# Kernel optimization log

Measured on AMD Instinct MI355X. Metric: run time of the kernel, lower is better.

Reference implementation:

```python
import jax, jax.numpy as jnp
import numpy as np

V, D, B, L = 433, 120, 4096, 16  # vocab, d_model, batch, seq_len
H4 = 4 * D
LN_EPS = 1e-5


def setup_inputs() -> dict:
    key = jax.random.key(0)
    ks = jax.random.split(key, 12)
    s = 1.0 / np.sqrt(D)  # PyTorch LSTM init range
    u = lambda k, shape: jax.random.uniform(k, shape, jnp.float32, -s, s)
    return {
        "x": jax.random.randint(ks[0], (B, L), 0, V, dtype=jnp.int32),
        "embed": jax.random.normal(ks[1], (V, D), jnp.float32) * 0.02,
        "Wih0": u(ks[2], (H4, D)), "Whh0": u(ks[3], (H4, D)),
        "bih0": u(ks[4], (H4,)), "bhh0": u(ks[5], (H4,)),
        "Wih1": u(ks[6], (H4, D)), "Whh1": u(ks[7], (H4, D)),
        "bih1": u(ks[8], (H4,)), "bhh1": u(ks[9], (H4,)),
        "gamma": jnp.ones((D,), jnp.float32),
        "beta": jnp.zeros((D,), jnp.float32),
    }


def _lstm_layer(x, Wih, Whh, bih, bhh):
    """One LSTM layer, batch_first input [B,L,D] -> [B,L,H]. PyTorch gate order i,f,g,o."""
    b, _, _ = x.shape
    h_dim = Whh.shape[1]
    # Precompute input contribution for all timesteps in one big GEMM.
    xg = jnp.einsum('bld,gd->blg', x, Wih) + bih + bhh  # [B,L,4H]

    def step(carry, g_t):
        h, c = carry
        gates = g_t + h @ Whh.T  # [B,4H]
        i, f, g, o = jnp.split(gates, 4, axis=-1)
        c = jax.nn.sigmoid(f) * c + jax.nn.sigmoid(i) * jnp.tanh(g)
        h = jax.nn.sigmoid(o) * jnp.tanh(c)
        return (h, c), h

    init = (jnp.zeros((b, h_dim), x.dtype), jnp.zeros((b, h_dim), x.dtype))
    _, hs = jax.lax.scan(step, init, jnp.swapaxes(xg, 0, 1))  # [L,B,H]
    return jnp.swapaxes(hs, 0, 1)


def _layernorm(h, gamma, beta):
    mu = jnp.mean(h, axis=-1, keepdims=True)
    var = jnp.mean(jnp.square(h - mu), axis=-1, keepdims=True)
    return (h - mu) / jnp.sqrt(var + LN_EPS) * gamma + beta


def reference(x, embed, Wih0, Whh0, bih0, bhh0, Wih1, Whh1, bih1, bhh1, gamma, beta):
    h = embed[x]                               # [B,L,D] token embedding
    h = _lstm_layer(h, Wih0, Whh0, bih0, bhh0)  # layer 0
    h = _lstm_layer(h, Wih1, Whh1, bih1, bhh1)  # layer 1
    out = _layernorm(h, gamma, beta)
    logits = jnp.einsum('bld,vd->blv', out, embed)  # tied-embedding head (no bias)
    return logits
```

## Files before the change

### kernel.cpp

```cpp
#include <hip/hip_runtime.h>


#define VSZ 433
#define DIM 120
#define BSZ 4096
#define SEQ 16
#define H4  480
#define MTOT (BSZ*SEQ)
#define KP  128
#define NPAD 448
#define TB  16
#define GP  484
#define HP  136

typedef unsigned int   u32;
typedef unsigned short u16;
typedef __attribute__((ext_vector_type(8))) short    v8bf;
typedef __attribute__((ext_vector_type(8))) _Float16 v8h;
typedef __attribute__((ext_vector_type(4))) float    v4f;

__device__ __forceinline__ float bf2f(u16 u){ union{u32 i;float f;}z; z.i=((u32)u)<<16; return z.f; }
__device__ __forceinline__ u16 f2bf(float f){
  union{float f;u32 u;}z; z.f=f;
  u32 u = z.u + 0x7fffu + ((z.u>>16)&1u);
  return (u16)(u>>16);
}

#define EW_OFF   0u
#define B1S_OFF  831488u
#define EMBP_OFF 833408u
#define HB0_OFF  948096u
#define H1N_OFF  17725312u

__global__ __launch_bounds__(512) void k_ew(const float* __restrict__ embed,
                                            const float* __restrict__ Wih0,
                                            const float* __restrict__ bih0,
                                            const float* __restrict__ bhh0,
                                            float* __restrict__ EW)
{
  __shared__ float e[DIM];
  const int v = blockIdx.x, tid = threadIdx.x;
  if (tid < DIM) e[tid] = embed[v*DIM + tid];
  __syncthreads();
  if (tid < H4) {
    float acc = bih0[tid] + bhh0[tid];
    #pragma unroll
    for (int k0 = 0; k0 < DIM; k0 += 4) {
      float4 w = *(const float4*)(Wih0 + tid*DIM + k0);
      acc = fmaf(e[k0+0], w.x, acc);
      acc = fmaf(e[k0+1], w.y, acc);
      acc = fmaf(e[k0+2], w.z, acc);
      acc = fmaf(e[k0+3], w.w, acc);
    }
    EW[v*H4 + tid] = acc;
  }
}

__global__ __launch_bounds__(256) void k_prep2(const float* __restrict__ embed,
                                               const float* __restrict__ bih1,
                                               const float* __restrict__ bhh1,
                                               u16* __restrict__ embP,
                                               float* __restrict__ b1s)
{
  const int idx = blockIdx.x*256 + threadIdx.x;
  if (idx < NPAD*KP) {
    int n = idx >> 7, k = idx & 127;
    embP[idx] = (n < VSZ && k < DIM) ? f2bf(embed[n*DIM + k]) : (u16)0;
  } else if (idx < NPAD*KP + H4) {
    int g = idx - NPAD*KP;
    b1s[g] = bih1[g] + bhh1[g];
  }
}

__global__ __launch_bounds__(512) void k_rec0(const float* __restrict__ Whh,
                                              const float* __restrict__ EW,
                                              const int* __restrict__ x,
                                              _Float16* __restrict__ hb0)
{
  __shared__ float gLs[TB][GP];
  __shared__ __align__(16) _Float16 hLh[TB][HP];
  __shared__ int xL[TB*SEQ];

  const int tid  = threadIdx.x;
  const int wave = tid >> 6, lane = tid & 63;
  const int cl   = lane & 15, quad = lane >> 4;
  const int b0   = blockIdx.x * TB;

  for (int i = tid; i < TB*SEQ; i += 512) xL[i] = x[b0*SEQ + i];
  for (int i = tid; i < TB*HP; i += 512) (&hLh[0][0])[i] = (_Float16)0.f;
  __syncthreads();

  v8h Bf[4][4];
  #pragma unroll
  for (int i = 0; i < 4; ++i) {
    const int nt = wave*4 + i;
    const bool vld = (nt < 30);
    const int n = vld ? nt*16 + cl : 0;
    #pragma unroll
    for (int kt = 0; kt < 4; ++kt) {
      const int k0 = kt*32 + quad*8;
      v8h f = {0,0,0,0,0,0,0,0};
      if (vld && k0 < DIM) {
        float4 q0 = *(const float4*)(Whh + n*DIM + k0);
        float4 q1 = *(const float4*)(Whh + n*DIM + k0 + 4);
        f[0]=(_Float16)q0.x; f[1]=(_Float16)q0.y; f[2]=(_Float16)q0.z; f[3]=(_Float16)q0.w;
        f[4]=(_Float16)q1.x; f[5]=(_Float16)q1.y; f[6]=(_Float16)q1.z; f[7]=(_Float16)q1.w;
      }
      Bf[i][kt] = f;
    }
  }

  float srcv[4][4];
  auto load_src = [&](int t) {
    #pragma unroll
    for (int i = 0; i < 4; ++i) {
      const int nt = wave*4 + i;
      if (nt < 30) {
        const int n = nt*16 + cl;
        #pragma unroll
        for (int r = 0; r < 4; ++r)
          srcv[i][r] = EW[(size_t)xL[(quad*4 + r)*SEQ + t]*H4 + n];
      }
    }
  };
  load_src(0);

  const int d  = tid % 120;
  const int rg = tid / 120;
  float C[4] = {0.f, 0.f, 0.f, 0.f};

  for (int t = 0; t < SEQ; ++t) {
    __syncthreads();
    v8h Af[4];
    #pragma unroll
    for (int kt = 0; kt < 4; ++kt)
      Af[kt] = *(const v8h*)&hLh[cl][kt*32 + quad*8];
    v4f acc[4];
    #pragma unroll
    for (int i = 0; i < 4; ++i) {
      acc[i][0]=srcv[i][0]; acc[i][1]=srcv[i][1];
      acc[i][2]=srcv[i][2]; acc[i][3]=srcv[i][3];
    }
    #pragma unroll
    for (int i = 0; i < 4; ++i)
      if (wave*4 + i < 30) {
        #pragma unroll
        for (int kt = 0; kt < 4; ++kt)
          acc[i] = __builtin_amdgcn_mfma_f32_16x16x32_f16(Af[kt], Bf[i][kt], acc[i], 0, 0, 0);
      }
    if (t + 1 < SEQ) load_src(t + 1);
    #pragma unroll
    for (int i = 0; i < 4; ++i) {
      const int nt = wave*4 + i;
      if (nt < 30) {
        #pragma unroll
        for (int r = 0; r < 4; ++r)
          gLs[quad*4 + r][nt*16 + cl] = acc[i][r];
      }
    }
    __syncthreads();
    if (tid < 480) {
      #pragma unroll
      for (int r = 0; r < 4; ++r) {
        const int row = rg*4 + r;
        const float gi = gLs[row][d      ];
        const float gf = gLs[row][d + 120];
        const float gg = gLs[row][d + 240];
        const float go = gLs[row][d + 360];
        const float si = 1.f / (1.f + __expf(-gi));
        const float sf = 1.f / (1.f + __expf(-gf));
        const float tg = 1.f - 2.f / (__expf(2.f*gg) + 1.f);
        const float so = 1.f / (1.f + __expf(-go));
        const float c  = sf * C[r] + si * tg;
        C[r] = c;
        const float tc = 1.f - 2.f / (__expf(2.f*c) + 1.f);
        const float h  = so * tc;
        hLh[row][d] = (_Float16)h;
        hb0[((size_t)t*BSZ + b0 + row)*KP + d] = (_Float16)h;
      }
    } else {
      const int i = tid - 480;
      #pragma unroll
      for (int j = 0; j < 4; ++j) {
        const int idx = i*4 + j, row = idx >> 3, col = 120 + (idx & 7);
        hb0[((size_t)t*BSZ + b0 + row)*KP + col] = (_Float16)0.f;
      }
    }
  }
}

__global__ __launch_bounds__(512) void k_rec1(const float* __restrict__ Wih1,
                                              const float* __restrict__ Whh1,
                                              const float* __restrict__ b1s,
                                              const _Float16* __restrict__ hb0,
                                              const float* __restrict__ gamma,
                                              const float* __restrict__ beta,
                                              u16* __restrict__ h1n)
{
  __shared__ float gLs[TB][GP];
  __shared__ __align__(16) _Float16 hLh[TB][HP];

  const int tid  = threadIdx.x;
  const int wave = tid >> 6, lane = tid & 63;
  const int cl   = lane & 15, quad = lane >> 4;
  const int b0   = blockIdx.x * TB;

  for (int i = tid; i < TB*HP; i += 512) (&hLh[0][0])[i] = (_Float16)0.f;

  v8h Bi[4][4], Bh[4][4];
  float bias[4];
  #pragma unroll
  for (int i = 0; i < 4; ++i) {
    const int nt = wave*4 + i;
    const bool vld = (nt < 30);
    const int n = vld ? nt*16 + cl : 0;
    bias[i] = vld ? b1s[n] : 0.f;
    #pragma unroll
    for (int kt = 0; kt < 4; ++kt) {
      const int k0 = kt*32 + quad*8;
      v8h fi = {0,0,0,0,0,0,0,0}, fh = {0,0,0,0,0,0,0,0};
      if (vld && k0 < DIM) {
        float4 q0 = *(const float4*)(Wih1 + n*DIM + k0);
        float4 q1 = *(const float4*)(Wih1 + n*DIM + k0 + 4);
        fi[0]=(_Float16)q0.x; fi[1]=(_Float16)q0.y; fi[2]=(_Float16)q0.z; fi[3]=(_Float16)q0.w;
        fi[4]=(_Float16)q1.x; fi[5]=(_Float16)q1.y; fi[6]=(_Float16)q1.z; fi[7]=(_Float16)q1.w;
        float4 p0 = *(const float4*)(Whh1 + n*DIM + k0);
        float4 p1 = *(const float4*)(Whh1 + n*DIM + k0 + 4);
        fh[0]=(_Float16)p0.x; fh[1]=(_Float16)p0.y; fh[2]=(_Float16)p0.z; fh[3]=(_Float16)p0.w;
        fh[4]=(_Float16)p1.x; fh[5]=(_Float16)p1.y; fh[6]=(_Float16)p1.z; fh[7]=(_Float16)p1.w;
      }
      Bi[i][kt] = fi;
      Bh[i][kt] = fh;
    }
  }

  const int d  = tid % 120;
  const int rg = tid / 120;
  const float gmm = (tid < 480) ? gamma[d] : 0.f;
  const float bta = (tid < 480) ? beta[d]  : 0.f;
  float C[4] = {0.f, 0.f, 0.f, 0.f};
  __syncthreads();

  for (int t = 0; t < SEQ; ++t) {
    v8h A0[4], A1[4];
    #pragma unroll
    for (int kt = 0; kt < 4; ++kt)
      A0[kt] = *(const v8h*)&hb0[((size_t)t*BSZ + b0 + cl)*KP + kt*32 + quad*8];
    #pragma unroll
    for (int kt = 0; kt < 4; ++kt)
      A1[kt] = *(const v8h*)&hLh[cl][kt*32 + quad*8];
    v4f acc[4];
    #pragma unroll
    for (int i = 0; i < 4; ++i)
      acc[i] = (v4f){bias[i], bias[i], bias[i], bias[i]};
    #pragma unroll
    for (int i = 0; i < 4; ++i)
      if (wave*4 + i < 30) {
        #pragma unroll
        for (int kt = 0; kt < 4; ++kt) {
          acc[i] = __builtin_amdgcn_mfma_f32_16x16x32_f16(A0[kt], Bi[i][kt], acc[i], 0, 0, 0);
          acc[i] = __builtin_amdgcn_mfma_f32_16x16x32_f16(A1[kt], Bh[i][kt], acc[i], 0, 0, 0);
        }
      }
    #pragma unroll
    for (int i = 0; i < 4; ++i) {
      const int nt = wave*4 + i;
      if (nt < 30) {
        #pragma unroll
        for (int r = 0; r < 4; ++r)
          gLs[quad*4 + r][nt*16 + cl] = acc[i][r];
      }
    }
    __syncthreads();
    float hreg[4];
    if (tid < 480) {
      #pragma unroll
      for (int r = 0; r < 4; ++r) {
        const int row = rg*4 + r;
        const float gi = gLs[row][d      ];
        const float gf = gLs[row][d + 120];
        const float gg = gLs[row][d + 240];
        const float go = gLs[row][d + 360];
        const float si = 1.f / (1.f + __expf(-gi));
        const float sf = 1.f / (1.f + __expf(-gf));
        const float tg = 1.f - 2.f / (__expf(2.f*gg) + 1.f);
        const float so = 1.f / (1.f + __expf(-go));
        const float c  = sf * C[r] + si * tg;
        C[r] = c;
        const float tc = 1.f - 2.f / (__expf(2.f*c) + 1.f);
        const float h  = so * tc;
        hreg[r] = h;
        hLh[row][d] = (_Float16)h;
        gLs[row][d] = h;
      }
    }
    __syncthreads();
    if (tid < 128) {
      const int row = tid >> 3, seg = tid & 7;
      float s1 = 0.f, s2 = 0.f;
      #pragma unroll
      for (int j = 0; j < 15; ++j) {
        const float v = gLs[row][seg*15 + j];
        s1 += v; s2 = fmaf(v, v, s2);
      }
      gLs[row][464 + seg] = s1;
      gLs[row][472 + seg] = s2;
    }
    __syncthreads();
    if (tid < 16) {
      float s1 = 0.f, s2 = 0.f;
      #pragma unroll
      for (int j = 0; j < 8; ++j) { s1 += gLs[tid][464 + j]; s2 += gLs[tid][472 + j]; }
      const float mu = s1 * (1.f/DIM);
      const float var = s2 * (1.f/DIM) - mu*mu;
      gLs[tid][480] = mu;
      gLs[tid][481] = rsqrtf(var + 1e-5f);
    }
    __syncthreads();
    if (tid < 480) {
      #pragma unroll
      for (int r = 0; r < 4; ++r) {
        const int row = rg*4 + r;
        const float mu = gLs[row][480], rs = gLs[row][481];
        const float v = fmaf((hreg[r] - mu)*rs, gmm, bta);
        h1n[((size_t)(b0 + row)*SEQ + t)*KP + d] = f2bf(v);
      }
    } else {
      const int i = tid - 480;
      #pragma unroll
      for (int j = 0; j < 4; ++j) {
        const int idx = i*4 + j, row = idx >> 3, col = 120 + (idx & 7);
        h1n[((size_t)(b0 + row)*SEQ + t)*KP + col] = (u16)0;
      }
    }
    __syncthreads();
  }
}

__global__ __launch_bounds__(256) void k_head(const u16* __restrict__ A,
                                              const u16* __restrict__ Bp,
                                              float* __restrict__ out)
{
  const int wv = threadIdx.x >> 6, lane = threadIdx.x & 63;
  const int cl = lane & 15, quad = lane >> 4;
  const int mtb = (blockIdx.x*4 + wv)*4;
  v8bf a[4][4];
  #pragma unroll
  for (int i = 0; i < 4; ++i)
    #pragma unroll
    for (int kt = 0; kt < 4; ++kt)
      a[i][kt] = *(const v8bf*)&A[((size_t)(mtb+i)*16 + cl)*KP + kt*32 + quad*8];
  for (int nt = 0; nt < NPAD/16; ++nt) {
    const int n = nt*16 + cl;
    v8bf bfr[4];
    #pragma unroll
    for (int kt = 0; kt < 4; ++kt)
      bfr[kt] = *(const v8bf*)&Bp[(size_t)n*KP + kt*32 + quad*8];
    #pragma unroll
    for (int i = 0; i < 4; ++i) {
      v4f acc = {0.f, 0.f, 0.f, 0.f};
      #pragma unroll
      for (int kt = 0; kt < 4; ++kt)
        acc = __builtin_amdgcn_mfma_f32_16x16x32_bf16(a[i][kt], bfr[kt], acc, 0, 0, 0);
      if (n < VSZ) {
        #pragma unroll
        for (int r = 0; r < 4; ++r)
          out[(size_t)((mtb+i)*16 + quad*4 + r)*VSZ + n] = acc[r];
      }
    }
  }
}

extern "C" void kernel_launch(void* const* d_in, const int* in_sizes, int n_in,
                              void* d_out, int out_size, void* d_ws, size_t ws_size,
                              hipStream_t stream)
{
  (void)in_sizes; (void)n_in; (void)out_size; (void)ws_size;
  const int*   x     = (const int*)d_in[0];
  const float* embed = (const float*)d_in[1];
  const float* Wih0  = (const float*)d_in[2];
  const float* Whh0  = (const float*)d_in[3];
  const float* bih0  = (const float*)d_in[4];
  const float* bhh0  = (const float*)d_in[5];
  const float* Wih1  = (const float*)d_in[6];
  const float* Whh1  = (const float*)d_in[7];
  const float* bih1  = (const float*)d_in[8];
  const float* bhh1  = (const float*)d_in[9];
  const float* gamma = (const float*)d_in[10];
  const float* beta  = (const float*)d_in[11];

  char* ws = (char*)d_ws;
  float*     EW   = (float*)(ws + EW_OFF);
  float*     b1s  = (float*)(ws + B1S_OFF);
  u16*       embP = (u16*)(ws + EMBP_OFF);
  _Float16*  hb0  = (_Float16*)(ws + HB0_OFF);
  u16*       h1n  = (u16*)(ws + H1N_OFF);

  k_ew   <<<VSZ, 512, 0, stream>>>(embed, Wih0, bih0, bhh0, EW);
  k_prep2<<<226, 256, 0, stream>>>(embed, bih1, bhh1, embP, b1s);
  k_rec0 <<<BSZ/TB, 512, 0, stream>>>(Whh0, EW, x, hb0);
  k_rec1 <<<BSZ/TB, 512, 0, stream>>>(Wih1, Whh1, b1s, hb0, gamma, beta, h1n);
  k_head <<<MTOT/256, 256, 0, stream>>>(h1n, embP, (float*)d_out);
}
```

Measured before the change: 296.0 us.

## Remap gate math to per-wave rows and use warp-shuffle LayerNorm reduction

Both recurrent kernels now give each wave two batch rows, with each lane handling two hidden units using float2 LDS reads and packed half stores. In layer 1 the LayerNorm statistics are reduced with wave-level xor shuffles instead of an LDS tree, which removes three block barriers per timestep. The next timestep's layer-0 hidden input is also prefetched into registers ahead of the MFMAs. This aims to cut synchronisation and LDS traffic in the serial timestep loop, at the cost of more registers.

```diff
diff --git a/kernel.cpp b/kernel.cpp
--- a/kernel.cpp
+++ b/kernel.cpp
@@ -25,6 +25,11 @@
   u32 u = z.u + 0x7fffu + ((z.u>>16)&1u);
   return (u16)(u>>16);
 }
+__device__ __forceinline__ u32 packh2(float a, float b){
+  union{_Float16 h[2]; u32 u;} z;
+  z.h[0] = (_Float16)a; z.h[1] = (_Float16)b;
+  return z.u;
+}
 
 #define EW_OFF   0u
 #define B1S_OFF  831488u
@@ -125,9 +130,10 @@
   };
   load_src(0);
 
-  const int d  = tid % 120;
-  const int rg = tid / 120;
-  float C[4] = {0.f, 0.f, 0.f, 0.f};
+  const int prow = wave*2;
+  const bool act = lane < 60;
+  const int d0   = lane*2;
+  float C[2][2] = {{0.f,0.f},{0.f,0.f}};
 
   for (int t = 0; t < SEQ; ++t) {
     __syncthreads();
@@ -159,31 +165,32 @@
       }
     }
     __syncthreads();
-    if (tid < 480) {
-      #pragma unroll
-      for (int r = 0; r < 4; ++r) {
-        const int row = rg*4 + r;
-        const float gi = gLs[row][d      ];
-        const float gf = gLs[row][d + 120];
-        const float gg = gLs[row][d + 240];
-        const float go = gLs[row][d + 360];
-        const float si = 1.f / (1.f + __expf(-gi));
-        const float sf = 1.f / (1.f + __expf(-gf));
-        const float tg = 1.f - 2.f / (__expf(2.f*gg) + 1.f);
-        const float so = 1.f / (1.f + __expf(-go));
-        const float c  = sf * C[r] + si * tg;
-        C[r] = c;
-        const float tc = 1.f - 2.f / (__expf(2.f*c) + 1.f);
-        const float h  = so * tc;
-        hLh[row][d] = (_Float16)h;
-        hb0[((size_t)t*BSZ + b0 + row)*KP + d] = (_Float16)h;
-      }
-    } else {
-      const int i = tid - 480;
-      #pragma unroll
-      for (int j = 0; j < 4; ++j) {
-        const int idx = i*4 + j, row = idx >> 3, col = 120 + (idx & 7);
-        hb0[((size_t)t*BSZ + b0 + row)*KP + col] = (_Float16)0.f;
+    #pragma unroll
+    for (int rr = 0; rr < 2; ++rr) {
+      const int row = prow + rr;
+      if (act) {
+        const float2 gi = *(const float2*)&gLs[row][d0      ];
+        const float2 gf = *(const float2*)&gLs[row][d0 + 120];
+        const float2 gg = *(const float2*)&gLs[row][d0 + 240];
+        const float2 go = *(const float2*)&gLs[row][d0 + 360];
+        float h2[2];
+        #pragma unroll
+        for (int k = 0; k < 2; ++k) {
+          const float vi = k ? gi.y : gi.x, vf = k ? gf.y : gf.x;
+          const float vg = k ? gg.y : gg.x, vo = k ? go.y : go.x;
+          const float si = 1.f / (1.f + __expf(-vi));
+          const float sf = 1.f / (1.f + __expf(-vf));
+          const float tg = 1.f - 2.f / (__expf(2.f*vg) + 1.f);
+          const float so = 1.f / (1.f + __expf(-vo));
+          const float c  = sf * C[rr][k] + si * tg;
+          C[rr][k] = c;
+          const float tc = 1.f - 2.f / (__expf(2.f*c) + 1.f);
+          h2[k] = so * tc;
+        }
+        *(u32*)&hLh[row][d0] = packh2(h2[0], h2[1]);
+        *(u32*)&hb0[((size_t)t*BSZ + b0 + row)*KP + d0] = packh2(h2[0], h2[1]);
+      } else {
+        *(u32*)&hb0[((size_t)t*BSZ + b0 + row)*KP + 120 + 2*(lane - 60)] = 0u;
       }
     }
   }
@@ -234,21 +241,34 @@
     }
   }
 
-  const int d  = tid % 120;
-  const int rg = tid / 120;
-  const float gmm = (tid < 480) ? gamma[d] : 0.f;
-  const float bta = (tid < 480) ? beta[d]  : 0.f;
-  float C[4] = {0.f, 0.f, 0.f, 0.f};
+  const int prow = wave*2;
+  const bool act = lane < 60;
+  const int d0   = lane*2;
+  float gmm[2] = {0.f, 0.f}, bta[2] = {0.f, 0.f};
+  if (act) {
+    gmm[0] = gamma[d0]; gmm[1] = gamma[d0+1];
+    bta[0] = beta[d0];  bta[1] = beta[d0+1];
+  }
+  float C[2][2] = {{0.f,0.f},{0.f,0.f}};
+
+  v8h A0n[4];
+  #pragma unroll
+  for (int kt = 0; kt < 4; ++kt)
+    A0n[kt] = *(const v8h*)&hb0[((size_t)0*BSZ + b0 + cl)*KP + kt*32 + quad*8];
   __syncthreads();
 
   for (int t = 0; t < SEQ; ++t) {
-    v8h A0[4], A1[4];
-    #pragma unroll
-    for (int kt = 0; kt < 4; ++kt)
-      A0[kt] = *(const v8h*)&hb0[((size_t)t*BSZ + b0 + cl)*KP + kt*32 + quad*8];
+    v8h A0c[4], A1[4];
+    #pragma unroll
+    for (int kt = 0; kt < 4; ++kt) A0c[kt] = A0n[kt];
     #pragma unroll
     for (int kt = 0; kt < 4; ++kt)
       A1[kt] = *(const v8h*)&hLh[cl][kt*32 + quad*8];
+    if (t + 1 < SEQ) {
+      #pragma unroll
+      for (int kt = 0; kt < 4; ++kt)
+        A0n[kt] = *(const v8h*)&hb0[((size_t)(t+1)*BSZ + b0 + cl)*KP + kt*32 + quad*8];
+    }
     v4f acc[4];
     #pragma unroll
     for (int i = 0; i < 4; ++i)
@@ -258,8 +278,8 @@
       if (wave*4 + i < 30) {
         #pragma unroll
         for (int kt = 0; kt < 4; ++kt) {
-          acc[i] = __builtin_amdgcn_mfma_f32_16x16x32_f16(A0[kt], Bi[i][kt], acc[i], 0, 0, 0);
-          acc[i] = __builtin_amdgcn_mfma_f32_16x16x32_f16(A1[kt], Bh[i][kt], acc[i], 0, 0, 0);
+          acc[i] = __builtin_amdgcn_mfma_f32_16x16x32_f16(A0c[kt], Bi[i][kt], acc[i], 0, 0, 0);
+          acc[i] = __builtin_amdgcn_mfma_f32_16x16x32_f16(A1[kt],  Bh[i][kt], acc[i], 0, 0, 0);
         }
       }
     #pragma unroll
@@ -272,65 +292,55 @@
       }
     }
     __syncthreads();
-    float hreg[4];
-    if (tid < 480) {
-      #pragma unroll
-      for (int r = 0; r < 4; ++r) {
-        const int row = rg*4 + r;
-        const float gi = gLs[row][d      ];
-        const float gf = gLs[row][d + 120];
-        const float gg = gLs[row][d + 240];
-        const float go = gLs[row][d + 360];
-        const float si = 1.f / (1.f + __expf(-gi));
-        const float sf = 1.f / (1.f + __expf(-gf));
-        const float tg = 1.f - 2.f / (__expf(2.f*gg) + 1.f);
-        const float so = 1.f / (1.f + __expf(-go));
-        const float c  = sf * C[r] + si * tg;
-        C[r] = c;
-        const float tc = 1.f - 2.f / (__expf(2.f*c) + 1.f);
-        const float h  = so * tc;
-        hreg[r] = h;
-        hLh[row][d] = (_Float16)h;
-        gLs[row][d] = h;
-      }
-    }
-    __syncthreads();
-    if (tid < 128) {
-      const int row = tid >> 3, seg = tid & 7;
-      float s1 = 0.f, s2 = 0.f;
-      #pragma unroll
-      for (int j = 0; j < 15; ++j) {
-        const float v = gLs[row][seg*15 + j];
-        s1 += v; s2 = fmaf(v, v, s2);
-      }
-      gLs[row][464 + seg] = s1;
-      gLs[row][472 + seg] = s2;
-    }
-    __syncthreads();
-    if (tid < 16) {
-      float s1 = 0.f, s2 = 0.f;
-      #pragma unroll
-      for (int j = 0; j < 8; ++j) { s1 += gLs[tid][464 + j]; s2 += gLs[tid][472 + j]; }
-      const float mu = s1 * (1.f/DIM);
-      const float var = s2 * (1.f/DIM) - mu*mu;
-      gLs[tid][480] = mu;
-      gLs[tid][481] = rsqrtf(var + 1e-5f);
-    }
-    __syncthreads();
-    if (tid < 480) {
-      #pragma unroll
-      for (int r = 0; r < 4; ++r) {
-        const int row = rg*4 + r;
-        const float mu = gLs[row][480], rs = gLs[row][481];
-        const float v = fmaf((hreg[r] - mu)*rs, gmm, bta);
-        h1n[((size_t)(b0 + row)*SEQ + t)*KP + d] = f2bf(v);
-      }
-    } else {
-      const int i = tid - 480;
-      #pragma unroll
-      for (int j = 0; j < 4; ++j) {
-        const int idx = i*4 + j, row = idx >> 3, col = 120 + (idx & 7);
-        h1n[((size_t)(b0 + row)*SEQ + t)*KP + col] = (u16)0;
+    float h2[2][2] = {{0.f,0.f},{0.f,0.f}};
+    float s1[2] = {0.f, 0.f}, s2[2] = {0.f, 0.f};
+    #pragma unroll
+    for (int rr = 0; rr < 2; ++rr) {
+      const int row = prow + rr;
+      if (act) {
+        const float2 gi = *(const float2*)&gLs[row][d0      ];
+        const float2 gf = *(const float2*)&gLs[row][d0 + 120];
+        const float2 gg = *(const float2*)&gLs[row][d0 + 240];
+        const float2 go = *(const float2*)&gLs[row][d0 + 360];
+        #pragma unroll
+        for (int k = 0; k < 2; ++k) {
+          const float vi = k ? gi.y : gi.x, vf = k ? gf.y : gf.x;
+          const float vg = k ? gg.y : gg.x, vo = k ? go.y : go.x;
+          const float si = 1.f / (1.f + __expf(-vi));
+          const float sf = 1.f / (1.f + __expf(-vf));
+          const float tg = 1.f - 2.f / (__expf(2.f*vg) + 1.f);
+          const float so = 1.f / (1.f + __expf(-vo));
+          const float c  = sf * C[rr][k] + si * tg;
+          C[rr][k] = c;
+          const float tc = 1.f - 2.f / (__expf(2.f*c) + 1.f);
+          const float h  = so * tc;
+          h2[rr][k] = h;
+          s1[rr] += h;
+          s2[rr] = fmaf(h, h, s2[rr]);
+        }
+        *(u32*)&hLh[row][d0] = packh2(h2[rr][0], h2[rr][1]);
+      }
+    }
+    #pragma unroll
+    for (int m = 32; m >= 1; m >>= 1) {
+      s1[0] += __shfl_xor(s1[0], m);
+      s2[0] += __shfl_xor(s2[0], m);
+      s1[1] += __shfl_xor(s1[1], m);
+      s2[1] += __shfl_xor(s2[1], m);
+    }
+    #pragma unroll
+    for (int rr = 0; rr < 2; ++rr) {
+      const int row = prow + rr;
+      const float mu = s1[rr] * (1.f/DIM);
+      const float var = s2[rr] * (1.f/DIM) - mu*mu;
+      const float rs = rsqrtf(var + 1e-5f);
+      u16* dst = &h1n[((size_t)(b0 + row)*SEQ + t)*KP];
+      if (act) {
+        const float v0 = fmaf((h2[rr][0] - mu)*rs, gmm[0], bta[0]);
+        const float v1 = fmaf((h2[rr][1] - mu)*rs, gmm[1], bta[1]);
+        *(u32*)&dst[d0] = (u32)f2bf(v0) | ((u32)f2bf(v1) << 16);
+      } else {
+        *(u32*)&dst[120 + 2*(lane - 60)] = 0u;
       }
     }
     __syncthreads();
```

New measurement: 288.1 us. 2.7% less time.
